# Kernel optimization log

Measured on AMD Instinct MI355X. Metric: run time of the kernel, lower is better.

The kernel has to match this reference:

```python
import jax, jax.numpy as jnp
import numpy as np

E = 8       # num_experts
TOP_K = 2
H = 512     # hidden_size
DFF = 2048  # expert FFN inner dim (4*H)
B, S = 4, 2048


def setup_inputs() -> dict:
    key = jax.random.key(0)
    k0, k1, k2, k3 = jax.random.split(key, 4)
    return {
        "hidden_states": jax.random.normal(k0, (B, S, H), jnp.float32),
        # router gate: kaiming-ish init scaled by 0.01 (near-uniform routing)
        "gate_w": jax.random.normal(k1, (E, H), jnp.float32) * 0.01,
        "w1": jax.random.normal(k2, (E, H, DFF), jnp.float32) * (1.0 / np.sqrt(H)),
        "b1": jnp.zeros((E, DFF), jnp.float32),
        "w2": jax.random.normal(k3, (E, DFF, H), jnp.float32) * (1.0 / np.sqrt(DFF)),
        "b2": jnp.zeros((E, H), jnp.float32),
    }


def reference(hidden_states, gate_w, w1, b1, w2, b2):
    # hidden_states: (B, S, H)
    b, s, h = hidden_states.shape
    flat = hidden_states.reshape(-1, h)                 # (T, H), T = B*S

    # --- TopKRouter (eval mode: no gaussian noise) ---
    logits = flat @ gate_w.T                            # (T, E)
    top_vals, top_idx = jax.lax.top_k(logits, TOP_K)    # (T, K)
    top_w = jax.nn.softmax(top_vals, axis=-1)           # softmax over selected k only

    # combine[t, e] = routing weight of expert e for token t (0 if not selected).
    # top_k indices are distinct per token, so summing over k matches the
    # original masked scatter-add output[mask] += weight * expert_out.
    combine = jnp.sum(
        jax.nn.one_hot(top_idx, E, dtype=flat.dtype) * top_w[..., None], axis=1
    )                                                   # (T, E)

    # --- experts: dense compute per expert, weighted combine ---
    out = jnp.zeros_like(flat)
    for e in range(E):  # fixed small loop over experts (not a data dim)
        hdn = jax.nn.gelu(flat @ w1[e] + b1[e])         # (T, DFF)
        out = out + combine[:, e:e + 1] * (hdn @ w2[e] + b2[e])
    return out.reshape(b, s, h)
```

## Files before the change

### kernel.cpp

```cpp
#include <hip/hip_runtime.h>
#include <hip/hip_bf16.h>

#define E_    8
#define H_    512
#define DFF_  2048
#define T_    8192
#define NSLOT (2 * T_)

typedef float  f32x4  __attribute__((ext_vector_type(4)));
typedef short  bf16x8 __attribute__((ext_vector_type(8)));

static __device__ __forceinline__ ushort f2bf(float f) {
  union { float f; unsigned u; } v; v.f = f;
  unsigned r = v.u + 0x7FFFu + ((v.u >> 16) & 1u);
  return (ushort)(r >> 16);
}

static __device__ __forceinline__ void gload16(const void* g, void* l) {
  __builtin_amdgcn_global_load_lds((const __attribute__((address_space(1))) void*)g,
                                   (__attribute__((address_space(3))) void*)l, 16, 0, 0);
}

static __device__ __forceinline__ void transpose_body(
    const float* __restrict__ in, ushort* __restrict__ out, int R, int C,
    int bx, int by, int e, float tile[64][65], int t) {
  int r0 = by * 64, c0 = bx * 64;
  int row = t >> 2, seg = t & 3;
  const float* src = in + ((size_t)e * R + r0 + row) * C + c0 + seg * 16;
#pragma unroll
  for (int i = 0; i < 4; ++i) {
    float4 v = *(const float4*)(src + i * 4);
    tile[row][seg * 16 + i * 4 + 0] = v.x;
    tile[row][seg * 16 + i * 4 + 1] = v.y;
    tile[row][seg * 16 + i * 4 + 2] = v.z;
    tile[row][seg * 16 + i * 4 + 3] = v.w;
  }
  __syncthreads();
  int c = t >> 2;
  ushort vals[16];
#pragma unroll
  for (int j = 0; j < 16; ++j) vals[j] = f2bf(tile[seg * 16 + j][c]);
  ushort* dst = out + ((size_t)e * C + c0 + c) * R + r0 + seg * 16;
  *(uint4*)(dst)     = *(uint4*)&vals[0];
  *(uint4*)(dst + 8) = *(uint4*)&vals[8];
}

__global__ void prep_kernel(const float* __restrict__ x, const float* __restrict__ gw,
                            const float* __restrict__ w1, const float* __restrict__ w2,
                            ushort* __restrict__ xb, float* __restrict__ slotw,
                            int* __restrict__ slote, ushort* __restrict__ w1t,
                            ushort* __restrict__ w2t, float* __restrict__ out) {
  __shared__ float tile[64][65];
  int bid = blockIdx.x;
  int tid = threadIdx.x;
  if (bid < 2048) {
    int tokn = bid * 4 + (tid >> 6);
    int lane = tid & 63;
    const float4* xr = (const float4*)(x + (size_t)tokn * H_ + lane * 8);
    float4 x0 = xr[0], x1 = xr[1];
    ushort v[8] = {f2bf(x0.x), f2bf(x0.y), f2bf(x0.z), f2bf(x0.w),
                   f2bf(x1.x), f2bf(x1.y), f2bf(x1.z), f2bf(x1.w)};
    *(uint4*)(xb + (size_t)tokn * H_ + lane * 8) = *(uint4*)v;
    float acc[E_];
#pragma unroll
    for (int e = 0; e < E_; ++e) {
      const float4* gr = (const float4*)(gw + e * H_ + lane * 8);
      float4 g0 = gr[0], g1 = gr[1];
      acc[e] = x0.x*g0.x + x0.y*g0.y + x0.z*g0.z + x0.w*g0.w
             + x1.x*g1.x + x1.y*g1.y + x1.z*g1.z + x1.w*g1.w;
    }
#pragma unroll
    for (int e = 0; e < E_; ++e) {
#pragma unroll
      for (int off = 32; off; off >>= 1)
        acc[e] += __shfl_xor(acc[e], off);
    }
    if (lane == 0) {
      float v1 = -1e30f, v2 = -1e30f; int i1 = 0, i2 = 0;
#pragma unroll
      for (int e = 0; e < E_; ++e) {
        float vv = acc[e];
        if (vv > v1)      { v2 = v1; i2 = i1; v1 = vv; i1 = e; }
        else if (vv > v2) { v2 = vv; i2 = e; }
      }
      float ex = expf(v2 - v1);
      float inv = 1.0f / (1.0f + ex);
      slote[2 * tokn] = i1;     slotw[2 * tokn] = inv;
      slote[2 * tokn + 1] = i2; slotw[2 * tokn + 1] = ex * inv;
    }
  } else if (bid < 4096) {
    float* p = out + (size_t)(bid - 2048) * 2048 + tid * 8;
    float4 z = {0.f, 0.f, 0.f, 0.f};
    *(float4*)(p) = z;
    *(float4*)(p + 4) = z;
  } else if (bid < 6144) {
    int blk = bid - 4096;
    int bx = blk & 31, by = (blk >> 5) & 7, e = blk >> 8;
    transpose_body(w1, w1t, H_, DFF_, bx, by, e, tile, tid);
  } else {
    int blk = bid - 6144;
    int bx = blk & 7, by = (blk >> 3) & 31, e = blk >> 8;
    transpose_body(w2, w2t, DFF_, H_, bx, by, e, tile, tid);
  }
}

__global__ __launch_bounds__(1024) void listbuild_kernel(
    const int* __restrict__ slote, int* __restrict__ counts, int* __restrict__ ebase,
    int* __restrict__ lslot) {
  int tid = threadIdx.x, lane = tid & 63, wv = tid >> 6;
  int base = tid * 16;
  int myexp[16];
  unsigned char cnt[E_] = {0, 0, 0, 0, 0, 0, 0, 0};
#pragma unroll
  for (int i = 0; i < 16; ++i) {
    int e = slote[base + i];
    myexp[i] = e;
    cnt[e]++;
  }
  unsigned long long lo = 0, hi = 0;
#pragma unroll
  for (int e = 0; e < 4; ++e) {
    lo |= (unsigned long long)cnt[e] << (16 * e);
    hi |= (unsigned long long)cnt[e + 4] << (16 * e);
  }
  unsigned long long mylo = lo, myhi = hi;
#pragma unroll
  for (int off = 1; off < 64; off <<= 1) {
    unsigned long long tl = __shfl_up(lo, off);
    unsigned long long th = __shfl_up(hi, off);
    if (lane >= off) { lo += tl; hi += th; }
  }
  __shared__ unsigned long long wtotlo[16], wtothi[16];
  __shared__ unsigned long long wbaselo[16], wbasehi[16];
  if (lane == 63) { wtotlo[wv] = lo; wtothi[wv] = hi; }
  __syncthreads();
  if (tid == 0) {
    unsigned long long rl = 0, rh = 0;
#pragma unroll
    for (int w2 = 0; w2 < 16; ++w2) {
      wbaselo[w2] = rl; wbasehi[w2] = rh;
      rl += wtotlo[w2]; rh += wtothi[w2];
    }
    int run = 0;
#pragma unroll
    for (int e = 0; e < 4; ++e) {
      int tot = (int)((rl >> (16 * e)) & 0xFFFF);
      counts[e] = tot; ebase[e] = run; run += tot;
    }
#pragma unroll
    for (int e = 0; e < 4; ++e) {
      int tot = (int)((rh >> (16 * e)) & 0xFFFF);
      counts[e + 4] = tot; ebase[e + 4] = run; run += tot;
    }
  }
  __syncthreads();
  unsigned long long exlo = wbaselo[wv] + lo - mylo;
  unsigned long long exhi = wbasehi[wv] + hi - myhi;
  int pos[E_];
#pragma unroll
  for (int e = 0; e < 4; ++e) {
    pos[e]     = (int)((exlo >> (16 * e)) & 0xFFFF);
    pos[e + 4] = (int)((exhi >> (16 * e)) & 0xFFFF);
  }
#pragma unroll
  for (int i = 0; i < 16; ++i) {
    int e = myexp[i];
    lslot[e * T_ + pos[e]] = base + i;
    pos[e]++;
  }
}

__global__ __launch_bounds__(256, 2) void gemm1_kernel(
    const ushort* __restrict__ xb, const ushort* __restrict__ w1t,
    const float* __restrict__ b1, const int* __restrict__ counts,
    const int* __restrict__ ebase, const int* __restrict__ lslot,
    ushort* __restrict__ hdn, int c0, int DC) {
  int bid = blockIdx.x;
  int e = bid & (E_ - 1);
  int nx = DC / 128;
  int bx = (bid >> 3) % nx;
  int by = (bid >> 3) / nx;
  int cnt = counts[e];
  int m0 = by * 64;
  if (m0 >= cnt) return;
  int n0 = c0 + bx * 128;
  int eb = ebase[e];

  __shared__ ushort sA[64 * 64];
  __shared__ ushort sB[128 * 64];
  int tid = threadIdx.x, lane = tid & 63, wid = tid >> 6;
  int wm = wid >> 1, wn = wid & 1;
  const int* lst = lslot + e * T_;
  const ushort* w1e = w1t + (size_t)e * DFF_ * H_;

  int lrow = lane >> 3;
  int scol = ((lane & 7) ^ lrow) * 8;

  const ushort* asrc[2]; const ushort* bsrc[4];
#pragma unroll
  for (int is = 0; is < 2; ++is) {
    int row = (wid * 2 + is) * 8 + lrow;
    int r = m0 + row; if (r > cnt - 1) r = cnt - 1;
    asrc[is] = xb + (size_t)(lst[r] >> 1) * H_ + scol;
  }
#pragma unroll
  for (int is = 0; is < 4; ++is) {
    int row = (wid * 4 + is) * 8 + lrow;
    bsrc[is] = w1e + (size_t)(n0 + row) * H_ + scol;
  }

  f32x4 acc[2][4];
#pragma unroll
  for (int i = 0; i < 2; ++i)
#pragma unroll
    for (int j = 0; j < 4; ++j) acc[i][j] = (f32x4){0.f, 0.f, 0.f, 0.f};

  for (int k0 = 0; k0 < H_; k0 += 64) {
    __syncthreads();
#pragma unroll
    for (int is = 0; is < 2; ++is)
      gload16(asrc[is] + k0, &sA[(wid * 2 + is) * 512]);
#pragma unroll
    for (int is = 0; is < 4; ++is)
      gload16(bsrc[is] + k0, &sB[(wid * 4 + is) * 512]);
    __syncthreads();
#pragma unroll
    for (int s = 0; s < 2; ++s) {
      bf16x8 af[2], bfr[4];
#pragma unroll
      for (int i = 0; i < 2; ++i) {
        int row = wm * 32 + i * 16 + (lane & 15);
        af[i] = *(const bf16x8*)(&sA[row * 64 + (((s * 4 + (lane >> 4)) ^ (row & 7)) * 8)]);
      }
#pragma unroll
      for (int j = 0; j < 4; ++j) {
        int row = wn * 64 + j * 16 + (lane & 15);
        bfr[j] = *(const bf16x8*)(&sB[row * 64 + (((s * 4 + (lane >> 4)) ^ (row & 7)) * 8)]);
      }
#pragma unroll
      for (int i = 0; i < 2; ++i)
#pragma unroll
        for (int j = 0; j < 4; ++j)
          acc[i][j] = __builtin_amdgcn_mfma_f32_16x16x32_bf16(af[i], bfr[j], acc[i][j], 0, 0, 0);
    }
  }

  int cl = lane & 15, rg = lane >> 4;
  float b1v[4];
#pragma unroll
  for (int j = 0; j < 4; ++j) b1v[j] = b1[e * DFF_ + n0 + wn * 64 + j * 16 + cl];
#pragma unroll
  for (int i = 0; i < 2; ++i) {
    int rbase = m0 + wm * 32 + i * 16 + rg * 4;
#pragma unroll
    for (int r = 0; r < 4; ++r) {
      int gr = rbase + r;
      if (gr < cnt) {
        ushort* hrow = hdn + (size_t)(eb + gr) * DC + (n0 - c0) + wn * 64 + cl;
#pragma unroll
        for (int j = 0; j < 4; ++j) {
          float v = acc[i][j][r] + b1v[j];
          float t2 = v + 0.044715f * v * v * v;
          float exv = __expf(1.5957691216057308f * t2);
          float th = 1.0f - 2.0f / (exv + 1.0f);
          hrow[j * 16] = f2bf(0.5f * v * (1.0f + th));
        }
      }
    }
  }
}

__global__ __launch_bounds__(256, 2) void gemm2_kernel(
    const ushort* __restrict__ hdn, const ushort* __restrict__ w2t,
    const float* __restrict__ b2, const float* __restrict__ slotw,
    const int* __restrict__ counts, const int* __restrict__ ebase,
    const int* __restrict__ lslot, float* __restrict__ out,
    int c0, int DC, int addb) {
  int bid = blockIdx.x;
  int e = bid & (E_ - 1);
  const int nx = H_ / 128;
  int bx = (bid >> 3) % nx;
  int by = (bid >> 3) / nx;
  int cnt = counts[e];
  int m0 = by * 64;
  if (m0 >= cnt) return;
  int n0 = bx * 128;
  int eb = ebase[e];

  __shared__ ushort sA[64 * 64];
  __shared__ ushort sB[128 * 64];
  int tid = threadIdx.x, lane = tid & 63, wid = tid >> 6;
  int wm = wid >> 1, wn = wid & 1;
  const int* lst = lslot + e * T_;
  const ushort* w2e = w2t + (size_t)e * H_ * DFF_ + c0;

  int lrow = lane >> 3;
  int scol = ((lane & 7) ^ lrow) * 8;

  const ushort* asrc[2]; const ushort* bsrc[4];
#pragma unroll
  for (int is = 0; is < 2; ++is) {
    int row = (wid * 2 + is) * 8 + lrow;
    int r = m0 + row; if (r > cnt - 1) r = cnt - 1;
    asrc[is] = hdn + (size_t)(eb + r) * DC + scol;
  }
#pragma unroll
  for (int is = 0; is < 4; ++is) {
    int row = (wid * 4 + is) * 8 + lrow;
    bsrc[is] = w2e + (size_t)(n0 + row) * DFF_ + scol;
  }

  f32x4 acc[2][4];
#pragma unroll
  for (int i = 0; i < 2; ++i)
#pragma unroll
    for (int j = 0; j < 4; ++j) acc[i][j] = (f32x4){0.f, 0.f, 0.f, 0.f};

  for (int k0 = 0; k0 < DC; k0 += 64) {
    __syncthreads();
#pragma unroll
    for (int is = 0; is < 2; ++is)
      gload16(asrc[is] + k0, &sA[(wid * 2 + is) * 512]);
#pragma unroll
    for (int is = 0; is < 4; ++is)
      gload16(bsrc[is] + k0, &sB[(wid * 4 + is) * 512]);
    __syncthreads();
#pragma unroll
    for (int s = 0; s < 2; ++s) {
      bf16x8 af[2], bfr[4];
#pragma unroll
      for (int i = 0; i < 2; ++i) {
        int row = wm * 32 + i * 16 + (lane & 15);
        af[i] = *(const bf16x8*)(&sA[row * 64 + (((s * 4 + (lane >> 4)) ^ (row & 7)) * 8)]);
      }
#pragma unroll
      for (int j = 0; j < 4; ++j) {
        int row = wn * 64 + j * 16 + (lane & 15);
        bfr[j] = *(const bf16x8*)(&sB[row * 64 + (((s * 4 + (lane >> 4)) ^ (row & 7)) * 8)]);
      }
#pragma unroll
      for (int i = 0; i < 2; ++i)
#pragma unroll
        for (int j = 0; j < 4; ++j)
          acc[i][j] = __builtin_amdgcn_mfma_f32_16x16x32_bf16(af[i], bfr[j], acc[i][j], 0, 0, 0);
    }
  }

  int cl = lane & 15, rg = lane >> 4;
  float b2v[4];
#pragma unroll
  for (int j = 0; j < 4; ++j)
    b2v[j] = addb ? b2[e * H_ + n0 + wn * 64 + j * 16 + cl] : 0.0f;
#pragma unroll
  for (int i = 0; i < 2; ++i) {
    int rbase = m0 + wm * 32 + i * 16 + rg * 4;
#pragma unroll
    for (int r = 0; r < 4; ++r) {
      int gr = rbase + r;
      if (gr < cnt) {
        int slot = lst[gr];
        float wgt = slotw[slot];
        float* orow = out + (size_t)(slot >> 1) * H_ + n0 + wn * 64 + cl;
#pragma unroll
        for (int j = 0; j < 4; ++j)
          atomicAdd(&orow[j * 16], wgt * (acc[i][j][r] + b2v[j]));
      }
    }
  }
}

extern "C" void kernel_launch(void* const* d_in, const int* in_sizes, int n_in,
                              void* d_out, int out_size, void* d_ws, size_t ws_size,
                              hipStream_t stream) {
  const float* x  = (const float*)d_in[0];
  const float* gw = (const float*)d_in[1];
  const float* w1 = (const float*)d_in[2];
  const float* b1 = (const float*)d_in[3];
  const float* w2 = (const float*)d_in[4];
  const float* b2 = (const float*)d_in[5];
  float* out = (float*)d_out;

  char* ws = (char*)d_ws;
  size_t off = 0;
  auto alloc = [&](size_t bytes) -> void* {
    void* p = ws + off; off += (bytes + 255) & ~(size_t)255; return p;
  };
  int*    counts = (int*)alloc(256);
  int*    ebase  = (int*)alloc(256);
  int*    lslot  = (int*)alloc((size_t)E_ * T_ * 4);
  float*  slotw  = (float*)alloc((size_t)NSLOT * 4);
  int*    slote  = (int*)alloc((size_t)NSLOT * 4);
  ushort* w1t    = (ushort*)alloc((size_t)E_ * DFF_ * H_ * 2);
  ushort* w2t    = (ushort*)alloc((size_t)E_ * H_ * DFF_ * 2);
  ushort* xb     = (ushort*)alloc((size_t)T_ * H_ * 2);

  int NC = 1;
  while (NC < 16 && off + (size_t)NSLOT * (DFF_ / NC) * 2 > ws_size) NC *= 2;
  int DC = DFF_ / NC;
  ushort* hdn = (ushort*)alloc((size_t)NSLOT * DC * 2);

  prep_kernel<<<8192, 256, 0, stream>>>(x, gw, w1, w2, xb, slotw, slote, w1t, w2t, out);
  listbuild_kernel<<<1, 1024, 0, stream>>>(slote, counts, ebase, lslot);

  for (int c = 0; c < NC; ++c) {
    gemm1_kernel<<<E_ * (DC / 128) * (T_ / 64), 256, 0, stream>>>(
        xb, w1t, b1, counts, ebase, lslot, hdn, c * DC, DC);
    gemm2_kernel<<<E_ * (H_ / 128) * (T_ / 64), 256, 0, stream>>>(
        hdn, w2t, b2, slotw, counts, ebase, lslot, out, c * DC, DC, c == NC - 1);
  }
}
```

Baseline: 158.5 us.

## Load A fragments directly from global into registers with one-step prefetch

Both expert GEMM kernels stop staging the token-activation (A) tile through shared memory. Each lane now loads its MFMA A fragments straight from global memory into registers and prefetches the next K step while the current one computes. This removes the LDS writes and reads for A and frees shared memory, which could allow higher occupancy. In exchange, the two warps that share the same rows now load that A data redundantly from global memory or cache, and per-lane gathered loads may coalesce less well than the bulk global-to-LDS copies.

```diff
diff --git a/kernel.cpp b/kernel.cpp
--- a/kernel.cpp
+++ b/kernel.cpp
@@ -186,7 +186,6 @@
   int n0 = c0 + bx * 128;
   int eb = ebase[e];
 
-  __shared__ ushort sA[64 * 64];
   __shared__ ushort sB[128 * 64];
   int tid = threadIdx.x, lane = tid & 63, wid = tid >> 6;
   int wm = wid >> 1, wn = wid & 1;
@@ -196,13 +195,14 @@
   int lrow = lane >> 3;
   int scol = ((lane & 7) ^ lrow) * 8;
 
-  const ushort* asrc[2]; const ushort* bsrc[4];
-#pragma unroll
-  for (int is = 0; is < 2; ++is) {
-    int row = (wid * 2 + is) * 8 + lrow;
-    int r = m0 + row; if (r > cnt - 1) r = cnt - 1;
-    asrc[is] = xb + (size_t)(lst[r] >> 1) * H_ + scol;
-  }
+  const ushort* arow[2];
+#pragma unroll
+  for (int i = 0; i < 2; ++i) {
+    int r = m0 + wm * 32 + i * 16 + (lane & 15);
+    if (r > cnt - 1) r = cnt - 1;
+    arow[i] = xb + (size_t)(lst[r] >> 1) * H_ + (lane >> 4) * 8;
+  }
+  const ushort* bsrc[4];
 #pragma unroll
   for (int is = 0; is < 4; ++is) {
     int row = (wid * 4 + is) * 8 + lrow;
@@ -215,23 +215,34 @@
 #pragma unroll
     for (int j = 0; j < 4; ++j) acc[i][j] = (f32x4){0.f, 0.f, 0.f, 0.f};
 
+  bf16x8 afn[2][2];
+#pragma unroll
+  for (int s = 0; s < 2; ++s)
+#pragma unroll
+    for (int i = 0; i < 2; ++i)
+      afn[s][i] = *(const bf16x8*)(arow[i] + s * 32);
+
   for (int k0 = 0; k0 < H_; k0 += 64) {
     __syncthreads();
 #pragma unroll
-    for (int is = 0; is < 2; ++is)
-      gload16(asrc[is] + k0, &sA[(wid * 2 + is) * 512]);
-#pragma unroll
     for (int is = 0; is < 4; ++is)
       gload16(bsrc[is] + k0, &sB[(wid * 4 + is) * 512]);
+    bf16x8 afc[2][2];
+#pragma unroll
+    for (int s = 0; s < 2; ++s)
+#pragma unroll
+      for (int i = 0; i < 2; ++i) afc[s][i] = afn[s][i];
+    if (k0 + 64 < H_) {
+#pragma unroll
+      for (int s = 0; s < 2; ++s)
+#pragma unroll
+        for (int i = 0; i < 2; ++i)
+          afn[s][i] = *(const bf16x8*)(arow[i] + k0 + 64 + s * 32);
+    }
     __syncthreads();
 #pragma unroll
     for (int s = 0; s < 2; ++s) {
-      bf16x8 af[2], bfr[4];
-#pragma unroll
-      for (int i = 0; i < 2; ++i) {
-        int row = wm * 32 + i * 16 + (lane & 15);
-        af[i] = *(const bf16x8*)(&sA[row * 64 + (((s * 4 + (lane >> 4)) ^ (row & 7)) * 8)]);
-      }
+      bf16x8 bfr[4];
 #pragma unroll
       for (int j = 0; j < 4; ++j) {
         int row = wn * 64 + j * 16 + (lane & 15);
@@ -241,7 +252,7 @@
       for (int i = 0; i < 2; ++i)
 #pragma unroll
         for (int j = 0; j < 4; ++j)
-          acc[i][j] = __builtin_amdgcn_mfma_f32_16x16x32_bf16(af[i], bfr[j], acc[i][j], 0, 0, 0);
+          acc[i][j] = __builtin_amdgcn_mfma_f32_16x16x32_bf16(afc[s][i], bfr[j], acc[i][j], 0, 0, 0);
     }
   }
 
@@ -287,7 +298,6 @@
   int n0 = bx * 128;
   int eb = ebase[e];
 
-  __shared__ ushort sA[64 * 64];
   __shared__ ushort sB[128 * 64];
   int tid = threadIdx.x, lane = tid & 63, wid = tid >> 6;
   int wm = wid >> 1, wn = wid & 1;
@@ -297,13 +307,14 @@
   int lrow = lane >> 3;
   int scol = ((lane & 7) ^ lrow) * 8;
 
-  const ushort* asrc[2]; const ushort* bsrc[4];
-#pragma unroll
-  for (int is = 0; is < 2; ++is) {
-    int row = (wid * 2 + is) * 8 + lrow;
-    int r = m0 + row; if (r > cnt - 1) r = cnt - 1;
-    asrc[is] = hdn + (size_t)(eb + r) * DC + scol;
-  }
+  const ushort* arow[2];
+#pragma unroll
+  for (int i = 0; i < 2; ++i) {
+    int r = m0 + wm * 32 + i * 16 + (lane & 15);
+    if (r > cnt - 1) r = cnt - 1;
+    arow[i] = hdn + (size_t)(eb + r) * DC + (lane >> 4) * 8;
+  }
+  const ushort* bsrc[4];
 #pragma unroll
   for (int is = 0; is < 4; ++is) {
     int row = (wid * 4 + is) * 8 + lrow;
@@ -316,23 +327,34 @@
 #pragma unroll
     for (int j = 0; j < 4; ++j) acc[i][j] = (f32x4){0.f, 0.f, 0.f, 0.f};
 
+  bf16x8 afn[2][2];
+#pragma unroll
+  for (int s = 0; s < 2; ++s)
+#pragma unroll
+    for (int i = 0; i < 2; ++i)
+      afn[s][i] = *(const bf16x8*)(arow[i] + s * 32);
+
   for (int k0 = 0; k0 < DC; k0 += 64) {
     __syncthreads();
 #pragma unroll
-    for (int is = 0; is < 2; ++is)
-      gload16(asrc[is] + k0, &sA[(wid * 2 + is) * 512]);
-#pragma unroll
     for (int is = 0; is < 4; ++is)
       gload16(bsrc[is] + k0, &sB[(wid * 4 + is) * 512]);
+    bf16x8 afc[2][2];
+#pragma unroll
+    for (int s = 0; s < 2; ++s)
+#pragma unroll
+      for (int i = 0; i < 2; ++i) afc[s][i] = afn[s][i];
+    if (k0 + 64 < DC) {
+#pragma unroll
+      for (int s = 0; s < 2; ++s)
+#pragma unroll
+        for (int i = 0; i < 2; ++i)
+          afn[s][i] = *(const bf16x8*)(arow[i] + k0 + 64 + s * 32);
+    }
     __syncthreads();
 #pragma unroll
     for (int s = 0; s < 2; ++s) {
-      bf16x8 af[2], bfr[4];
-#pragma unroll
-      for (int i = 0; i < 2; ++i) {
-        int row = wm * 32 + i * 16 + (lane & 15);
-        af[i] = *(const bf16x8*)(&sA[row * 64 + (((s * 4 + (lane >> 4)) ^ (row & 7)) * 8)]);
-      }
+      bf16x8 bfr[4];
 #pragma unroll
       for (int j = 0; j < 4; ++j) {
         int row = wn * 64 + j * 16 + (lane & 15);
@@ -342,7 +364,7 @@
       for (int i = 0; i < 2; ++i)
 #pragma unroll
         for (int j = 0; j < 4; ++j)
-          acc[i][j] = __builtin_amdgcn_mfma_f32_16x16x32_bf16(af[i], bfr[j], acc[i][j], 0, 0, 0);
+          acc[i][j] = __builtin_amdgcn_mfma_f32_16x16x32_bf16(afc[s][i], bfr[j], acc[i][j], 0, 0, 0);
     }
   }
 
```

Result: slower. 235.2 us (+48.4%).

## Double-buffer LDS tiles in gemm2 to overlap global loads with MFMA

Applied to the files above, without the earlier changes.

Splits the gemm2 shared-memory tiles into two ping-pong buffers. The main K loop now prefetches the next 64-wide chunk with async global_load_lds while the current chunk feeds the MFMAs. Explicit vmcnt waits and raw barriers replace the pair of __syncthreads per step, so the kernel no longer stalls on each tile load before computing. In exchange LDS use per block doubles, and the loop assumes the number of K chunks is even.

```diff
diff --git a/kernel.cpp b/kernel.cpp
--- a/kernel.cpp
+++ b/kernel.cpp
@@ -287,8 +287,10 @@
   int n0 = bx * 128;
   int eb = ebase[e];
 
-  __shared__ ushort sA[64 * 64];
-  __shared__ ushort sB[128 * 64];
+  __shared__ ushort sA0[64 * 64];
+  __shared__ ushort sB0[128 * 64];
+  __shared__ ushort sA1[64 * 64];
+  __shared__ ushort sB1[128 * 64];
   int tid = threadIdx.x, lane = tid & 63, wid = tid >> 6;
   int wm = wid >> 1, wn = wid & 1;
   const int* lst = lslot + e * T_;
@@ -316,35 +318,59 @@
 #pragma unroll
     for (int j = 0; j < 4; ++j) acc[i][j] = (f32x4){0.f, 0.f, 0.f, 0.f};
 
-  for (int k0 = 0; k0 < DC; k0 += 64) {
-    __syncthreads();
-#pragma unroll
-    for (int is = 0; is < 2; ++is)
-      gload16(asrc[is] + k0, &sA[(wid * 2 + is) * 512]);
-#pragma unroll
-    for (int is = 0; is < 4; ++is)
-      gload16(bsrc[is] + k0, &sB[(wid * 4 + is) * 512]);
-    __syncthreads();
-#pragma unroll
-    for (int s = 0; s < 2; ++s) {
-      bf16x8 af[2], bfr[4];
-#pragma unroll
-      for (int i = 0; i < 2; ++i) {
-        int row = wm * 32 + i * 16 + (lane & 15);
-        af[i] = *(const bf16x8*)(&sA[row * 64 + (((s * 4 + (lane >> 4)) ^ (row & 7)) * 8)]);
-      }
-#pragma unroll
-      for (int j = 0; j < 4; ++j) {
-        int row = wn * 64 + j * 16 + (lane & 15);
-        bfr[j] = *(const bf16x8*)(&sB[row * 64 + (((s * 4 + (lane >> 4)) ^ (row & 7)) * 8)]);
-      }
-#pragma unroll
-      for (int i = 0; i < 2; ++i)
-#pragma unroll
-        for (int j = 0; j < 4; ++j)
-          acc[i][j] = __builtin_amdgcn_mfma_f32_16x16x32_bf16(af[i], bfr[j], acc[i][j], 0, 0, 0);
-    }
-  }
+#define STG2(bA, bB, kk)                                                    \
+  {                                                                         \
+    int k0_ = (kk);                                                         \
+    _Pragma("unroll")                                                       \
+    for (int is = 0; is < 2; ++is)                                          \
+      gload16(asrc[is] + k0_, &bA[(wid * 2 + is) * 512]);                   \
+    _Pragma("unroll")                                                       \
+    for (int is = 0; is < 4; ++is)                                          \
+      gload16(bsrc[is] + k0_, &bB[(wid * 4 + is) * 512]);                   \
+  }
+
+#define CMP2(bA, bB)                                                        \
+  {                                                                         \
+    _Pragma("unroll")                                                       \
+    for (int s = 0; s < 2; ++s) {                                           \
+      bf16x8 af[2], bfr[4];                                                 \
+      _Pragma("unroll")                                                     \
+      for (int i = 0; i < 2; ++i) {                                         \
+        int row = wm * 32 + i * 16 + (lane & 15);                           \
+        af[i] = *(const bf16x8*)(&bA[row * 64 + (((s * 4 + (lane >> 4)) ^ (row & 7)) * 8)]); \
+      }                                                                     \
+      _Pragma("unroll")                                                     \
+      for (int j = 0; j < 4; ++j) {                                         \
+        int row = wn * 64 + j * 16 + (lane & 15);                           \
+        bfr[j] = *(const bf16x8*)(&bB[row * 64 + (((s * 4 + (lane >> 4)) ^ (row & 7)) * 8)]); \
+      }                                                                     \
+      _Pragma("unroll")                                                     \
+      for (int i = 0; i < 2; ++i)                                           \
+        _Pragma("unroll")                                                   \
+        for (int j = 0; j < 4; ++j)                                         \
+          acc[i][j] = __builtin_amdgcn_mfma_f32_16x16x32_bf16(af[i], bfr[j], acc[i][j], 0, 0, 0); \
+    }                                                                       \
+  }
+
+  const int nt = DC / 64;
+  STG2(sA0, sB0, 0);
+  STG2(sA1, sB1, 64);
+  for (int t = 0; t < nt; t += 2) {
+    if (t + 1 < nt) { asm volatile("s_waitcnt vmcnt(6)" ::: "memory"); }
+    else            { asm volatile("s_waitcnt vmcnt(0)" ::: "memory"); }
+    __builtin_amdgcn_s_barrier();
+    CMP2(sA0, sB0);
+    __builtin_amdgcn_s_barrier();
+    if (t + 2 < nt) STG2(sA0, sB0, (t + 2) * 64);
+    if (t + 2 < nt) { asm volatile("s_waitcnt vmcnt(6)" ::: "memory"); }
+    else            { asm volatile("s_waitcnt vmcnt(0)" ::: "memory"); }
+    __builtin_amdgcn_s_barrier();
+    CMP2(sA1, sB1);
+    __builtin_amdgcn_s_barrier();
+    if (t + 3 < nt) STG2(sA1, sB1, (t + 3) * 64);
+  }
+#undef STG2
+#undef CMP2
 
   int cl = lane & 15, rg = lane >> 4;
   float b2v[4];
```

Measured after the change: 157.9 us. No clear change (-0.4%).
